# Performance work log

Hardware: AMD Instinct MI355X
Metric: run time of the kernel (lower is better)

## Reference

```python
import jax, jax.numpy as jnp
import numpy as np

N, F, E, LIN, C, B = 16384, 500, 128, 128, 10, 4096
P_EDGE = 0.002  # ~32 avg degree


def _l2norm(x):
    # F.normalize(dim=1), eps=1e-12
    n = jnp.linalg.norm(x, axis=1, keepdims=True)
    return x / jnp.maximum(n, 1e-12)


def setup_inputs() -> dict:
    key = jax.random.key(0)
    ks = jax.random.split(key, 10)
    adj = (jax.random.uniform(ks[0], (N, N)) < P_EDGE).astype(jnp.float32)
    idx = jnp.arange(N)
    adj = adj.at[idx, idx].set(1.0)  # self-loops guarantee degree >= 1
    data = jax.random.normal(ks[1], (N, F), dtype=jnp.float32)
    nodes = jax.random.randint(ks[2], (B,), 0, N)
    # Encoder 1: Linear(2F -> E); Encoder 2: Linear(2E -> E); classifier heads
    W1 = jax.random.normal(ks[3], (E, 2 * F), dtype=jnp.float32) * 0.03
    b1 = jnp.zeros((E,), jnp.float32)
    W2 = jax.random.normal(ks[4], (E, 2 * E), dtype=jnp.float32) * 0.06
    b2 = jnp.zeros((E,), jnp.float32)
    Wl1 = jax.random.normal(ks[5], (LIN, E), dtype=jnp.float32) * 0.08
    bl1 = jnp.zeros((LIN,), jnp.float32)
    Wl2 = jax.random.normal(ks[6], (C, LIN), dtype=jnp.float32) * 0.12
    bl2 = jnp.zeros((C,), jnp.float32)
    return {"nodes": nodes, "adj": adj, "data": data,
            "W1": W1, "b1": b1, "W2": W2, "b2": b2,
            "Wl1": Wl1, "bl1": bl1, "Wl2": Wl2, "bl2": bl2}


def reference(nodes, adj, data, W1, b1, W2, b2, Wl1, bl1, Wl2, bl2):
    deg = jnp.sum(adj, axis=1, keepdims=True)  # [N,1]
    # Layer 1 (mean aggregator over full neighbor set): computed for all nodes
    neigh1 = (adj @ data) / deg                               # [N,F]
    h1 = jnp.concatenate([data, neigh1], axis=1)              # [N,2F] (self, neigh)
    H1 = _l2norm(jax.nn.relu(h1 @ W1.T + b1))                 # [N,E]
    # Layer 2: only for the queried node batch
    neigh2 = (adj[nodes] @ H1) / deg[nodes]                   # [B,E]
    h2 = jnp.concatenate([H1[nodes], neigh2], axis=1)         # [B,2E]
    H2 = _l2norm(jax.nn.relu(h2 @ W2.T + b2))                 # [B,E]
    x = H2 @ Wl1.T + bl1                                      # [B,LIN]
    x = x @ Wl2.T + bl2                                       # [B,C]
    return jax.nn.softmax(x, axis=1)
```

## Files before the change

kernel.cpp:

```cpp
#include <hip/hip_runtime.h>
#include <math.h>
#include <stddef.h>

#define N_NODES 16384
#define F_DIM   500
#define E_DIM   128
#define C_DIM   10
#define B_DIM   4096
#define MAXDEG  128

typedef __attribute__((ext_vector_type(8))) short short8;
typedef __attribute__((ext_vector_type(4))) float f32x4;

__device__ inline unsigned short f2bf(float f) {
    union { float f; unsigned int u; } v; v.f = f;
    unsigned int u = v.u;
    u += 0x7FFFu + ((u >> 16) & 1u);
    return (unsigned short)(u >> 16);
}
__device__ inline float bf2f(unsigned short u) {
    union { unsigned int u; float f; } v; v.u = (unsigned int)u << 16;
    return v.f;
}
__device__ inline short8 cvt8(float4 a, float4 b) {
    short8 v;
    v[0] = (short)f2bf(a.x); v[1] = (short)f2bf(a.y);
    v[2] = (short)f2bf(a.z); v[3] = (short)f2bf(a.w);
    v[4] = (short)f2bf(b.x); v[5] = (short)f2bf(b.y);
    v[6] = (short)f2bf(b.z); v[7] = (short)f2bf(b.w);
    return v;
}

__global__ __launch_bounds__(256) void k_prep1(const float* __restrict__ data,
                                               const float* __restrict__ W1,
                                               const float* __restrict__ W2,
                                               const float* __restrict__ Wl1,
                                               unsigned short* __restrict__ Xb16,
                                               unsigned short* __restrict__ W2ab16,
                                               unsigned short* __restrict__ W2bb16,
                                               float* __restrict__ Wl1t) {
    __shared__ float tile[32][33];
    const int bb = blockIdx.x;
    const int tid = threadIdx.x;

    if (bb < 64) {
        int idx = bb * 256 + tid;
        int n = idx >> 7, k = idx & 127;
        W2ab16[idx] = f2bf(W2[(size_t)n * 256 + k]);
        return;
    } else if (bb < 128) {
        int idx = (bb - 64) * 256 + tid;
        int n = idx >> 7, k = idx & 127;
        W2bb16[idx] = f2bf(W2[(size_t)n * 256 + 128 + k]);
        return;
    } else if (bb < 144) {
        int tb = bb - 128;
        int k0 = (tb & 3) * 32, e0 = (tb >> 2) * 32;
        int tx = tid & 31, ty0 = tid >> 5;
#pragma unroll
        for (int q = 0; q < 4; ++q) {
            int ty = ty0 + q * 8;
            tile[ty][tx] = Wl1[(size_t)(e0 + ty) * 128 + k0 + tx];
        }
        __syncthreads();
#pragma unroll
        for (int q = 0; q < 4; ++q) {
            int ty = ty0 + q * 8;
            Wl1t[(size_t)(k0 + ty) * 128 + e0 + tx] = tile[tx][ty];
        }
        return;
    }
    const int g = bb - 144;
    const int blockM = g * 32;
    const int w    = tid >> 6;
    const int lane = tid & 63;
    const int l16  = lane & 15;
    const int quad = lane >> 4;
    f32x4 acc[2][4] = {};
#pragma unroll 2
    for (int c = 0; c < 16; ++c) {
        const int kq = (c << 5) + quad * 8;
        const bool ok0 = (kq + 4 <= F_DIM);
        const bool ok1 = (kq + 8 <= F_DIM);
        short8 af[2], bfr[4];
#pragma unroll
        for (int mt = 0; mt < 2; ++mt) {
            const float* ap = data + (size_t)(blockM + mt * 16 + l16) * F_DIM + kq;
            float4 f0 = ok0 ? *(const float4*)ap       : make_float4(0.f, 0.f, 0.f, 0.f);
            float4 f1 = ok1 ? *(const float4*)(ap + 4) : make_float4(0.f, 0.f, 0.f, 0.f);
            af[mt] = cvt8(f0, f1);
        }
#pragma unroll
        for (int nt = 0; nt < 4; ++nt) {
            int n = w * 64 + nt * 16 + l16;
            const float* bp = W1 + (size_t)(n & 127) * 1000 + (n >> 7) * F_DIM + kq;
            float4 g0 = ok0 ? *(const float4*)bp       : make_float4(0.f, 0.f, 0.f, 0.f);
            float4 g1 = ok1 ? *(const float4*)(bp + 4) : make_float4(0.f, 0.f, 0.f, 0.f);
            bfr[nt] = cvt8(g0, g1);
        }
#pragma unroll
        for (int mt = 0; mt < 2; ++mt)
#pragma unroll
            for (int nt = 0; nt < 4; ++nt)
                acc[mt][nt] = __builtin_amdgcn_mfma_f32_16x16x32_bf16(af[mt], bfr[nt], acc[mt][nt], 0, 0, 0);
    }
#pragma unroll
    for (int mt = 0; mt < 2; ++mt)
#pragma unroll
        for (int nt = 0; nt < 4; ++nt) {
            int col = w * 64 + nt * 16 + l16;
#pragma unroll
            for (int r = 0; r < 4; ++r) {
                int row = blockM + mt * 16 + quad * 4 + r;
                Xb16[(size_t)row * 256 + col] = f2bf(acc[mt][nt][r]);
            }
        }
}

__global__ __launch_bounds__(256) void k_scan_gather(const float* __restrict__ adj,
                                                     const unsigned short* __restrict__ Xb16,
                                                     const float* __restrict__ b1,
                                                     unsigned short* __restrict__ nbr,
                                                     int* __restrict__ deg,
                                                     unsigned short* __restrict__ H1b) {
    const int i = blockIdx.x;
    const int tid = threadIdx.x;
    __shared__ int s_cnt;
    __shared__ int s_idx[MAXDEG];
    __shared__ float s_part[8][128];
    __shared__ float s_w[2];

    const float4* row4 = (const float4*)(adj + (size_t)i * N_NODES);
    if (tid == 0) s_cnt = 0;
    __syncthreads();
    float4 v[16];
#pragma unroll
    for (int p = 0; p < 16; ++p) v[p] = row4[p * 256 + tid];
#pragma unroll
    for (int p = 0; p < 16; ++p) {
        int col = p * 1024 + tid * 4;
        if (v[p].x != 0.f) { int q = atomicAdd(&s_cnt, 1); if (q < MAXDEG) s_idx[q] = col;     }
        if (v[p].y != 0.f) { int q = atomicAdd(&s_cnt, 1); if (q < MAXDEG) s_idx[q] = col + 1; }
        if (v[p].z != 0.f) { int q = atomicAdd(&s_cnt, 1); if (q < MAXDEG) s_idx[q] = col + 2; }
        if (v[p].w != 0.f) { int q = atomicAdd(&s_cnt, 1); if (q < MAXDEG) s_idx[q] = col + 3; }
    }
    __syncthreads();
    int cnt = s_cnt; if (cnt > MAXDEG) cnt = MAXDEG;
    if (tid < cnt) nbr[(size_t)i * MAXDEG + tid] = (unsigned short)s_idx[tid];
    if (tid == 0) deg[i] = cnt;

    const int g = tid >> 5, l = tid & 31;
    float4 a4 = make_float4(0.f, 0.f, 0.f, 0.f);
    for (int k = g; k < cnt; k += 8) {
        ushort4 x4 = ((const ushort4*)(Xb16 + (size_t)s_idx[k] * 256 + 128))[l];
        a4.x += bf2f(x4.x); a4.y += bf2f(x4.y); a4.z += bf2f(x4.z); a4.w += bf2f(x4.w);
    }
    *(float4*)&s_part[g][l * 4] = a4;
    __syncthreads();
    float vv = 0.f;
    if (tid < 128) {
        float tot = 0.f;
#pragma unroll
        for (int g2 = 0; g2 < 8; ++g2) tot += s_part[g2][tid];
        vv = bf2f(Xb16[(size_t)i * 256 + tid]) + tot / (float)cnt + b1[tid];
        vv = fmaxf(vv, 0.f);
        float s = vv * vv;
#pragma unroll
        for (int off = 32; off > 0; off >>= 1) s += __shfl_down(s, off, 64);
        if ((tid & 63) == 0) s_w[tid >> 6] = s;
    }
    __syncthreads();
    if (tid < 128) {
        float denom = fmaxf(sqrtf(s_w[0] + s_w[1]), 1e-12f);
        H1b[(size_t)i * 128 + tid] = f2bf(vv / denom);
    }
}

__global__ __launch_bounds__(256) void k_gemm2(const unsigned short* __restrict__ H1b,
                                               const unsigned short* __restrict__ W2bb16,
                                               const unsigned short* __restrict__ W2ab16,
                                               const int* __restrict__ nodes,
                                               unsigned short* __restrict__ Yb16,
                                               float* __restrict__ Ya) {
    const int bb = blockIdx.x;
    const bool selfp = (bb >= 512);
    const unsigned short* B = selfp ? W2ab16 : W2bb16;
    const int blockM = (selfp ? (bb - 512) : bb) * 32;
    const int tid  = threadIdx.x;
    const int w    = tid >> 6;
    const int lane = tid & 63;
    const int l16  = lane & 15;
    const int quad = lane >> 4;
    int rsrc0 = blockM + l16,      rsrc1 = blockM + 16 + l16;
    if (selfp) { rsrc0 = nodes[rsrc0]; rsrc1 = nodes[rsrc1]; }
    short8 af[2][4], bfr[2][4];
#pragma unroll
    for (int c = 0; c < 4; ++c) {
        af[0][c] = *(const short8*)(H1b + (size_t)rsrc0 * 128 + c * 32 + quad * 8);
        af[1][c] = *(const short8*)(H1b + (size_t)rsrc1 * 128 + c * 32 + quad * 8);
    }
#pragma unroll
    for (int nt = 0; nt < 2; ++nt) {
        int n = w * 32 + nt * 16 + l16;
#pragma unroll
        for (int c = 0; c < 4; ++c)
            bfr[nt][c] = *(const short8*)(B + (size_t)n * 128 + c * 32 + quad * 8);
    }
    f32x4 acc[2][2] = {};
#pragma unroll
    for (int c = 0; c < 4; ++c)
#pragma unroll
        for (int mt = 0; mt < 2; ++mt)
#pragma unroll
            for (int nt = 0; nt < 2; ++nt)
                acc[mt][nt] = __builtin_amdgcn_mfma_f32_16x16x32_bf16(af[mt][c], bfr[nt][c], acc[mt][nt], 0, 0, 0);
#pragma unroll
    for (int mt = 0; mt < 2; ++mt)
#pragma unroll
        for (int nt = 0; nt < 2; ++nt) {
            int col = w * 32 + nt * 16 + l16;
#pragma unroll
            for (int r = 0; r < 4; ++r) {
                int row = blockM + mt * 16 + quad * 4 + r;
                if (selfp) Ya[(size_t)row * 128 + col] = acc[mt][nt][r];
                else       Yb16[(size_t)row * 128 + col] = f2bf(acc[mt][nt][r]);
            }
        }
}

__global__ __launch_bounds__(256) void k_l2head(const int* __restrict__ nodes,
                                                const unsigned short* __restrict__ nbr,
                                                const int* __restrict__ deg,
                                                const unsigned short* __restrict__ Yb16,
                                                const float* __restrict__ Ya,
                                                const float* __restrict__ b2,
                                                const float* __restrict__ Wl1t,
                                                const float* __restrict__ bl1,
                                                const float* __restrict__ Wl2,
                                                const float* __restrict__ bl2,
                                                float* __restrict__ out) {
    const int lane = threadIdx.x & 63;
    const int b = blockIdx.x * 4 + (threadIdx.x >> 6);
    const int n = nodes[b];
    const int cnt = deg[n];
    const int myn  = (lane < cnt)      ? (int)nbr[(size_t)n * MAXDEG + lane]      : 0;
    const int myn2 = (lane + 64 < cnt) ? (int)nbr[(size_t)n * MAXDEG + lane + 64] : 0;
    const int half = lane >> 5, l32 = lane & 31;
    float ax = 0.f, ay = 0.f, az = 0.f, aw = 0.f;
    for (int k = half; k < cnt; k += 2) {
        int kk = k & 63;
        int j1 = __shfl(myn, kk);
        int j2 = __shfl(myn2, kk);
        int j = (k < 64) ? j1 : j2;
        ushort4 y4 = *(const ushort4*)(Yb16 + (size_t)j * 128 + l32 * 4);
        ax += bf2f(y4.x); ay += bf2f(y4.y); az += bf2f(y4.z); aw += bf2f(y4.w);
    }
    ax += __shfl_xor(ax, 32); ay += __shfl_xor(ay, 32);
    az += __shfl_xor(az, 32); aw += __shfl_xor(aw, 32);
    float4 ya = *(const float4*)(Ya + (size_t)b * 128 + l32 * 4);
    float4 bb = *(const float4*)(b2 + l32 * 4);
    float fc = (float)cnt;
    float h0 = fmaxf(ya.x + ax / fc + bb.x, 0.f);
    float h1 = fmaxf(ya.y + ay / fc + bb.y, 0.f);
    float h2 = fmaxf(ya.z + az / fc + bb.z, 0.f);
    float h3 = fmaxf(ya.w + aw / fc + bb.w, 0.f);
    float s = h0 * h0 + h1 * h1 + h2 * h2 + h3 * h3;
#pragma unroll
    for (int off = 16; off > 0; off >>= 1) s += __shfl_xor(s, off);
    float rden = 1.0f / fmaxf(sqrtf(s), 1e-12f);
    h0 *= rden; h1 *= rden; h2 *= rden; h3 *= rden;
    float2 bl = *(const float2*)(bl1 + 2 * lane);
    float x0 = bl.x, x1 = bl.y;
    const float* wl = Wl1t + 2 * lane;
    for (int m = 0; m < 32; ++m) {
        float k0 = __shfl(h0, m), k1 = __shfl(h1, m), k2 = __shfl(h2, m), k3 = __shfl(h3, m);
        float2 w0 = *(const float2*)(wl + (size_t)(m * 4 + 0) * 128);
        float2 w1 = *(const float2*)(wl + (size_t)(m * 4 + 1) * 128);
        float2 w2 = *(const float2*)(wl + (size_t)(m * 4 + 2) * 128);
        float2 w3 = *(const float2*)(wl + (size_t)(m * 4 + 3) * 128);
        x0 += k0 * w0.x + k1 * w1.x + k2 * w2.x + k3 * w3.x;
        x1 += k0 * w0.y + k1 * w1.y + k2 * w2.y + k3 * w3.y;
    }
    float cv[C_DIM];
#pragma unroll
    for (int cc = 0; cc < C_DIM; ++cc) {
        float2 w = *(const float2*)(Wl2 + (size_t)cc * 128 + 2 * lane);
        float p = x0 * w.x + x1 * w.y;
#pragma unroll
        for (int off = 32; off > 0; off >>= 1) p += __shfl_xor(p, off);
        cv[cc] = p + bl2[cc];
    }
    float mx = cv[0];
#pragma unroll
    for (int cc = 1; cc < C_DIM; ++cc) mx = fmaxf(mx, cv[cc]);
    float se = 0.f;
#pragma unroll
    for (int cc = 0; cc < C_DIM; ++cc) { cv[cc] = expf(cv[cc] - mx); se += cv[cc]; }
    float rse = 1.0f / se;
    float o = cv[0];
#pragma unroll
    for (int cc = 1; cc < C_DIM; ++cc) o = (lane == cc) ? cv[cc] : o;
    if (lane < C_DIM) out[(size_t)b * C_DIM + lane] = o * rse;
}

extern "C" void kernel_launch(void* const* d_in, const int* in_sizes, int n_in,
                              void* d_out, int out_size, void* d_ws, size_t ws_size,
                              hipStream_t stream) {
    const int*   nodes = (const int*)  d_in[0];
    const float* adj   = (const float*)d_in[1];
    const float* data  = (const float*)d_in[2];
    const float* W1    = (const float*)d_in[3];
    const float* b1    = (const float*)d_in[4];
    const float* W2    = (const float*)d_in[5];
    const float* b2    = (const float*)d_in[6];
    const float* Wl1   = (const float*)d_in[7];
    const float* bl1   = (const float*)d_in[8];
    const float* Wl2   = (const float*)d_in[9];
    const float* bl2   = (const float*)d_in[10];
    float* out = (float*)d_out;

    float* Wl1t = (float*)d_ws;
    float* Ya   = Wl1t + 16384;
    unsigned short* W2ab16 = (unsigned short*)(Ya + (size_t)B_DIM * 128);
    unsigned short* W2bb16 = W2ab16 + 16384;
    unsigned short* Xb16   = W2bb16 + 16384;
    unsigned short* H1b    = Xb16 + (size_t)N_NODES * 256;
    unsigned short* Yb16   = H1b + (size_t)N_NODES * 128;
    unsigned short* nbr    = Yb16 + (size_t)N_NODES * 128;
    int* deg = (int*)(nbr + (size_t)N_NODES * MAXDEG);

    k_prep1<<<656, 256, 0, stream>>>(data, W1, W2, Wl1,
                                     Xb16, W2ab16, W2bb16, Wl1t);
    k_scan_gather<<<N_NODES, 256, 0, stream>>>(adj, Xb16, b1, nbr, deg, H1b);
    k_gemm2<<<512 + 128, 256, 0, stream>>>(H1b, W2bb16, W2ab16, nodes, Yb16, Ya);
    k_l2head<<<B_DIM / 4, 256, 0, stream>>>(nodes, nbr, deg, Yb16, Ya, b2,
                                            Wl1t, bl1, Wl2, bl2, out);
}
```

Baseline: 1.434 ms.

## Split adjacency scan from gather and overlap it with the layer-1 GEMM

```diff
diff --git a/kernel.cpp b/kernel.cpp
--- a/kernel.cpp
+++ b/kernel.cpp
@@ -22,39 +22,69 @@
     union { unsigned int u; float f; } v; v.u = (unsigned int)u << 16;
     return v.f;
 }
-__device__ inline short8 cvt8(float4 a, float4 b) {
-    short8 v;
-    v[0] = (short)f2bf(a.x); v[1] = (short)f2bf(a.y);
-    v[2] = (short)f2bf(a.z); v[3] = (short)f2bf(a.w);
-    v[4] = (short)f2bf(b.x); v[5] = (short)f2bf(b.y);
-    v[6] = (short)f2bf(b.z); v[7] = (short)f2bf(b.w);
-    return v;
-}
-
-__global__ __launch_bounds__(256) void k_prep1(const float* __restrict__ data,
+
+__global__ __launch_bounds__(256) void k_front(const float* __restrict__ adj,
+                                               const float* __restrict__ data,
                                                const float* __restrict__ W1,
                                                const float* __restrict__ W2,
                                                const float* __restrict__ Wl1,
+                                               unsigned short* __restrict__ nbr,
+                                               int* __restrict__ deg,
                                                unsigned short* __restrict__ Xb16,
                                                unsigned short* __restrict__ W2ab16,
                                                unsigned short* __restrict__ W2bb16,
                                                float* __restrict__ Wl1t) {
-    __shared__ float tile[32][33];
     const int bb = blockIdx.x;
     const int tid = threadIdx.x;
 
-    if (bb < 64) {
-        int idx = bb * 256 + tid;
+    if (bb < 4096) {
+        const int lane = tid & 63;
+        const int row = bb * 4 + (tid >> 6);
+        const float4* r4 = (const float4*)(adj + (size_t)row * N_NODES);
+        const size_t nb = (size_t)row * MAXDEG;
+        const unsigned long long lowm = ~0ull >> (64 - lane - 1) >> 1;
+        int base = 0;
+#define PROC1(val, cix) do {                                                  \
+        bool p = (val) != 0.f;                                                \
+        unsigned long long m = __ballot(p);                                   \
+        if (p) {                                                              \
+            int pos = base + (int)__popcll(m & lowm);                         \
+            if (pos < MAXDEG) nbr[nb + pos] = (unsigned short)(cix);          \
+        }                                                                     \
+        base += (int)__popcll(m);                                             \
+    } while (0)
+#define PROC4(vv, tt) do {                                                    \
+        int colb = ((tt) * 64 + lane) * 4;                                    \
+        PROC1((vv).x, colb);                                                  \
+        PROC1((vv).y, colb + 1);                                              \
+        PROC1((vv).z, colb + 2);                                              \
+        PROC1((vv).w, colb + 3);                                              \
+    } while (0)
+        float4 cur = r4[lane];
+#pragma unroll 4
+        for (int t = 0; t < 63; ++t) {
+            float4 nxt = r4[(t + 1) * 64 + lane];
+            PROC4(cur, t);
+            cur = nxt;
+        }
+        PROC4(cur, 63);
+#undef PROC4
+#undef PROC1
+        if (lane == 0) deg[row] = (base > MAXDEG) ? MAXDEG : base;
+        return;
+    } else if (bb < 4160) {
+        int idx = (bb - 4096) * 256 + tid;
         int n = idx >> 7, k = idx & 127;
         W2ab16[idx] = f2bf(W2[(size_t)n * 256 + k]);
         return;
-    } else if (bb < 128) {
-        int idx = (bb - 64) * 256 + tid;
+    } else if (bb < 4224) {
+        int idx = (bb - 4160) * 256 + tid;
         int n = idx >> 7, k = idx & 127;
         W2bb16[idx] = f2bf(W2[(size_t)n * 256 + 128 + k]);
         return;
-    } else if (bb < 144) {
-        int tb = bb - 128;
+    } else if (bb < 4240) {
+        __shared__ float tile[32][33];
+        int tb = bb - 4224;
         int k0 = (tb & 3) * 32, e0 = (tb >> 2) * 32;
         int tx = tid & 31, ty0 = tid >> 5;
 #pragma unroll
@@ -70,39 +100,54 @@
         }
         return;
     }
-    const int g = bb - 144;
+    __shared__ unsigned short sA[32 * 40];
+    __shared__ unsigned short sB[256 * 40];
+    const int g = bb - 4240;
     const int blockM = g * 32;
     const int w    = tid >> 6;
     const int lane = tid & 63;
     const int l16  = lane & 15;
     const int quad = lane >> 4;
     f32x4 acc[2][4] = {};
-#pragma unroll 2
+#pragma unroll 1
     for (int c = 0; c < 16; ++c) {
-        const int kq = (c << 5) + quad * 8;
-        const bool ok0 = (kq + 4 <= F_DIM);
-        const bool ok1 = (kq + 8 <= F_DIM);
+        const int k0 = c << 5;
+        {
+            int row = tid >> 3, ch = tid & 7;
+            int k = k0 + ch * 4;
+            const float* p = data + (size_t)(blockM + row) * F_DIM + k;
+            float4 f = (k + 4 <= F_DIM) ? *(const float4*)p
+                                        : make_float4(0.f, 0.f, 0.f, 0.f);
+            ushort4 u;
+            u.x = f2bf(f.x); u.y = f2bf(f.y); u.z = f2bf(f.z); u.w = f2bf(f.w);
+            *(ushort4*)(sA + row * 40 + ch * 4) = u;
+        }
+#pragma unroll
+        for (int q = 0; q < 8; ++q) {
+            int idx = tid + 256 * q;
+            int row = idx >> 3, ch = idx & 7;
+            int k = k0 + ch * 4;
+            const float* p = W1 + (size_t)(row & 127) * 1000 + (row >> 7) * F_DIM + k;
+            float4 f = (k + 4 <= F_DIM) ? *(const float4*)p
+                                        : make_float4(0.f, 0.f, 0.f, 0.f);
+            ushort4 u;
+            u.x = f2bf(f.x); u.y = f2bf(f.y); u.z = f2bf(f.z); u.w = f2bf(f.w);
+            *(ushort4*)(sB + row * 40 + ch * 4) = u;
+        }
+        __syncthreads();
         short8 af[2], bfr[4];
 #pragma unroll
-        for (int mt = 0; mt < 2; ++mt) {
-            const float* ap = data + (size_t)(blockM + mt * 16 + l16) * F_DIM + kq;
-            float4 f0 = ok0 ? *(const float4*)ap       : make_float4(0.f, 0.f, 0.f, 0.f);
-            float4 f1 = ok1 ? *(const float4*)(ap + 4) : make_float4(0.f, 0.f, 0.f, 0.f);
-            af[mt] = cvt8(f0, f1);
-        }
-#pragma unroll
-        for (int nt = 0; nt < 4; ++nt) {
-            int n = w * 64 + nt * 16 + l16;
-            const float* bp = W1 + (size_t)(n & 127) * 1000 + (n >> 7) * F_DIM + kq;
-            float4 g0 = ok0 ? *(const float4*)bp       : make_float4(0.f, 0.f, 0.f, 0.f);
-            float4 g1 = ok1 ? *(const float4*)(bp + 4) : make_float4(0.f, 0.f, 0.f, 0.f);
-            bfr[nt] = cvt8(g0, g1);
-        }
+        for (int mt = 0; mt < 2; ++mt)
+            af[mt] = *(const short8*)(sA + (mt * 16 + l16) * 40 + quad * 8);
+#pragma unroll
+        for (int nt = 0; nt < 4; ++nt)
+            bfr[nt] = *(const short8*)(sB + (w * 64 + nt * 16 + l16) * 40 + quad * 8);
 #pragma unroll
         for (int mt = 0; mt < 2; ++mt)
 #pragma unroll
             for (int nt = 0; nt < 4; ++nt)
                 acc[mt][nt] = __builtin_amdgcn_mfma_f32_16x16x32_bf16(af[mt], bfr[nt], acc[mt][nt], 0, 0, 0);
+        __syncthreads();
     }
 #pragma unroll
     for (int mt = 0; mt < 2; ++mt)
@@ -117,39 +162,20 @@
         }
 }
 
-__global__ __launch_bounds__(256) void k_scan_gather(const float* __restrict__ adj,
-                                                     const unsigned short* __restrict__ Xb16,
-                                                     const float* __restrict__ b1,
-                                                     unsigned short* __restrict__ nbr,
-                                                     int* __restrict__ deg,
-                                                     unsigned short* __restrict__ H1b) {
+__global__ __launch_bounds__(256) void k_gather(const unsigned short* __restrict__ nbr,
+                                                const int* __restrict__ deg,
+                                                const unsigned short* __restrict__ Xb16,
+                                                const float* __restrict__ b1,
+                                                unsigned short* __restrict__ H1b) {
     const int i = blockIdx.x;
-    const int tid = threadIdx.x;
-    __shared__ int s_cnt;
+    const int t = threadIdx.x;
+    const int cnt = deg[i];
     __shared__ int s_idx[MAXDEG];
     __shared__ float s_part[8][128];
     __shared__ float s_w[2];
-
-    const float4* row4 = (const float4*)(adj + (size_t)i * N_NODES);
-    if (tid == 0) s_cnt = 0;
+    if (t < cnt) s_idx[t] = nbr[(size_t)i * MAXDEG + t];
     __syncthreads();
-    float4 v[16];
-#pragma unroll
-    for (int p = 0; p < 16; ++p) v[p] = row4[p * 256 + tid];
-#pragma unroll
-    for (int p = 0; p < 16; ++p) {
-        int col = p * 1024 + tid * 4;
-        if (v[p].x != 0.f) { int q = atomicAdd(&s_cnt, 1); if (q < MAXDEG) s_idx[q] = col;     }
-        if (v[p].y != 0.f) { int q = atomicAdd(&s_cnt, 1); if (q < MAXDEG) s_idx[q] = col + 1; }
-        if (v[p].z != 0.f) { int q = atomicAdd(&s_cnt, 1); if (q < MAXDEG) s_idx[q] = col + 2; }
-        if (v[p].w != 0.f) { int q = atomicAdd(&s_cnt, 1); if (q < MAXDEG) s_idx[q] = col + 3; }
-    }
-    __syncthreads();
-    int cnt = s_cnt; if (cnt > MAXDEG) cnt = MAXDEG;
-    if (tid < cnt) nbr[(size_t)i * MAXDEG + tid] = (unsigned short)s_idx[tid];
-    if (tid == 0) deg[i] = cnt;
-
-    const int g = tid >> 5, l = tid & 31;
+    const int g = t >> 5, l = t & 31;
     float4 a4 = make_float4(0.f, 0.f, 0.f, 0.f);
     for (int k = g; k < cnt; k += 8) {
         ushort4 x4 = ((const ushort4*)(Xb16 + (size_t)s_idx[k] * 256 + 128))[l];
@@ -158,21 +184,21 @@
     *(float4*)&s_part[g][l * 4] = a4;
     __syncthreads();
     float vv = 0.f;
-    if (tid < 128) {
+    if (t < 128) {
         float tot = 0.f;
 #pragma unroll
-        for (int g2 = 0; g2 < 8; ++g2) tot += s_part[g2][tid];
-        vv = bf2f(Xb16[(size_t)i * 256 + tid]) + tot / (float)cnt + b1[tid];
+        for (int g2 = 0; g2 < 8; ++g2) tot += s_part[g2][t];
+        vv = bf2f(Xb16[(size_t)i * 256 + t]) + tot / (float)cnt + b1[t];
         vv = fmaxf(vv, 0.f);
         float s = vv * vv;
 #pragma unroll
         for (int off = 32; off > 0; off >>= 1) s += __shfl_down(s, off, 64);
-        if ((tid & 63) == 0) s_w[tid >> 6] = s;
+        if ((t & 63) == 0) s_w[t >> 6] = s;
     }
     __syncthreads();
-    if (tid < 128) {
+    if (t < 128) {
         float denom = fmaxf(sqrtf(s_w[0] + s_w[1]), 1e-12f);
-        H1b[(size_t)i * 128 + tid] = f2bf(vv / denom);
+        H1b[(size_t)i * 128 + t] = f2bf(vv / denom);
     }
 }
 
@@ -329,9 +355,10 @@
     unsigned short* nbr    = Yb16 + (size_t)N_NODES * 128;
     int* deg = (int*)(nbr + (size_t)N_NODES * MAXDEG);
 
-    k_prep1<<<656, 256, 0, stream>>>(data, W1, W2, Wl1,
-                                     Xb16, W2ab16, W2bb16, Wl1t);
-    k_scan_gather<<<N_NODES, 256, 0, stream>>>(adj, Xb16, b1, nbr, deg, H1b);
+    k_front<<<4096 + 144 + 512, 256, 0, stream>>>(adj, data, W1, W2, Wl1,
+                                                  nbr, deg, Xb16,
+                                                  W2ab16, W2bb16, Wl1t);
+    k_gather<<<N_NODES, 256, 0, stream>>>(nbr, deg, Xb16, b1, H1b);
     k_gemm2<<<512 + 128, 256, 0, stream>>>(H1b, W2bb16, W2ab16, nodes, Yb16, Ya);
     k_l2head<<<B_DIM / 4, 256, 0, stream>>>(nodes, nbr, deg, Yb16, Ya, b2,
                                             Wl1t, bl1, Wl2, bl2, out);
```

Measured after the change: 1.461 ms. No clear change (+1.9%).
